# Kernel tuning notes

Measured on AMD Instinct MI355X. Metric: run time of the kernel, lower is better.

## Reference

```python
import jax, jax.numpy as jnp
import numpy as np

B, S, D, H = 4, 1024, 1024, 16
HD = D // H  # head_dim = 64


def setup_inputs() -> dict:
    key = jax.random.key(0)
    ks = jax.random.split(key, 12)
    std = 1.0 / np.sqrt(D)
    inp = {
        "query": jax.random.normal(ks[0], (B, S, D), jnp.float32),
        "key": jax.random.normal(ks[1], (B, S, D), jnp.float32),
        "value": jax.random.normal(ks[2], (B, S, D), jnp.float32),
        # four Linear(embed_dim, embed_dim) layers: q, k, v, out
        "Wq": jax.random.normal(ks[3], (D, D), jnp.float32) * std,
        "bq": jnp.zeros((D,), jnp.float32),
        "Wk": jax.random.normal(ks[4], (D, D), jnp.float32) * std,
        "bk": jnp.zeros((D,), jnp.float32),
        "Wv": jax.random.normal(ks[5], (D, D), jnp.float32) * std,
        "bv": jnp.zeros((D,), jnp.float32),
        "Wo": jax.random.normal(ks[6], (D, D), jnp.float32) * std,
        "bo": jnp.zeros((D,), jnp.float32),
        # compressor: Linear(num_heads, 1)
        "Wc": jax.random.normal(ks[7], (H,), jnp.float32) / np.sqrt(H),
        "bc": jnp.zeros((), jnp.float32),
    }
    return inp


def reference(query, key, value, Wq, bq, Wk, bk, Wv, bv, Wo, bo, Wc, bc):
    b, s, d = query.shape
    h, hd = H, HD

    def proj(x, W, bias):
        # [b,s,d] @ [d,d] -> [b,h,s,hd]
        y = jnp.einsum('bsd,de->bse', x, W) + bias
        return y.reshape(b, s, h, hd).transpose(0, 2, 1, 3)

    q = proj(query, Wq, bq)
    k = proj(key, Wk, bk)
    v = proj(value, Wv, bv)

    scores = jnp.einsum('bhqd,bhkd->bhqk', q, k) / np.sqrt(hd)
    p_attn = jax.nn.softmax(scores, axis=-1)  # [b,h,s,s]; dropout is identity in eval

    x = jnp.einsum('bhqk,bhkd->bhqd', p_attn, v)
    x = x.transpose(0, 2, 1, 3).reshape(b, s, d)
    out = jnp.einsum('bsd,de->bse', x, Wo) + bo

    # head compression: Linear(num_heads, 1) over head axis -> [b,1,s,s]
    attn_c = (jnp.einsum('bhqk,h->bqk', p_attn, Wc) + bc)[:, None, :, :]
    return out, attn_c
```

## Files before the change

### kernel.cpp

```cpp
#include <hip/hip_runtime.h>
#include <hip/hip_bf16.h>

#define SS 1024
#define DD 1024
#define HH 16
#define HDh 64

typedef short bf16x8 __attribute__((ext_vector_type(8)));
typedef float f32x4 __attribute__((ext_vector_type(4)));

__device__ inline unsigned short f2bf(float f) {
    union { __hip_bfloat16 h; unsigned short u; } cv;
    cv.h = __float2bfloat16(f);
    return cv.u;
}
__device__ inline float bf2f(short u) {
    unsigned int x = ((unsigned int)(unsigned short)u) << 16;
    return __uint_as_float(x);
}

#define PIN4(a, b, c, d) asm volatile("" : "+v"(a), "+v"(b), "+v"(c), "+v"(d))

__device__ inline void gload_lds16(const unsigned short* g, unsigned short* l) {
    __builtin_amdgcn_global_load_lds(
        (const __attribute__((address_space(1))) unsigned int*)g,
        (__attribute__((address_space(3))) unsigned int*)l, 16, 0, 0);
}

__global__ __launch_bounds__(256) void prep(
    const float* __restrict__ a, const float* __restrict__ b, const float* __restrict__ c,
    unsigned short* __restrict__ oa, unsigned short* __restrict__ ob, unsigned short* __restrict__ oc,
    const float* __restrict__ Wq, const float* __restrict__ Wk,
    const float* __restrict__ Wv, const float* __restrict__ Wo,
    unsigned short* __restrict__ oq, unsigned short* __restrict__ okk,
    unsigned short* __restrict__ ov, unsigned short* __restrict__ oo)
{
    __shared__ float tile[32][33];
    int bid = blockIdx.x;
    if (bid < 4096) {
        size_t i = ((size_t)bid * 256 + threadIdx.x) * 4;
        float4 va = *(const float4*)(a + i);
        float4 vb = *(const float4*)(b + i);
        float4 vc = *(const float4*)(c + i);
        *(ushort4*)(oa + i) = make_ushort4(f2bf(va.x), f2bf(va.y), f2bf(va.z), f2bf(va.w));
        *(ushort4*)(ob + i) = make_ushort4(f2bf(vb.x), f2bf(vb.y), f2bf(vb.z), f2bf(vb.w));
        *(ushort4*)(oc + i) = make_ushort4(f2bf(vc.x), f2bf(vc.y), f2bf(vc.z), f2bf(vc.w));
    } else {
        int idx = bid - 4096;
        int z = idx >> 10;
        const float* W = z == 0 ? Wq : (z == 1 ? Wk : (z == 2 ? Wv : Wo));
        unsigned short* O = z == 0 ? oq : (z == 1 ? okk : (z == 2 ? ov : oo));
        int e0 = (idx & 31) * 32, d0 = ((idx >> 5) & 31) * 32;
        int r = threadIdx.x >> 3, c4 = (threadIdx.x & 7) * 4;
        float4 v = *(const float4*)(W + (size_t)(d0 + r) * DD + e0 + c4);
        tile[r][c4 + 0] = v.x; tile[r][c4 + 1] = v.y; tile[r][c4 + 2] = v.z; tile[r][c4 + 3] = v.w;
        __syncthreads();
        ushort4 u = make_ushort4(f2bf(tile[c4 + 0][r]), f2bf(tile[c4 + 1][r]),
                                 f2bf(tile[c4 + 2][r]), f2bf(tile[c4 + 3][r]));
        *(ushort4*)(O + (size_t)(e0 + r) * DD + d0 + c4) = u;
    }
}

__device__ inline void gemm128_core(const unsigned short* __restrict__ A,
                                    const unsigned short* __restrict__ Bt,
                                    const float* __restrict__ bias,
                                    void* __restrict__ out, int mode, float oscale,
                                    int m0, int n0)
{
    __shared__ unsigned short As[128 * 64];
    __shared__ unsigned short Bs[128 * 64];
    int t = threadIdx.x;
    int w = t >> 6, lane = t & 63, quad = lane >> 4, l15 = lane & 15;
    int wm = w >> 1, wn = w & 1;

    f32x4 zero = {0.f, 0.f, 0.f, 0.f};
    f32x4 acc[4][4];
#pragma unroll
    for (int i = 0; i < 4; i++)
#pragma unroll
        for (int j = 0; j < 4; j++) acc[i][j] = zero;

    for (int k0 = 0; k0 < DD; k0 += 64) {
        __syncthreads();
#pragma unroll
        for (int i = 0; i < 8; i++) {
            int chunk = w + i * 4;
            int half = chunk >> 4;
            int sub = chunk & 15;
            const unsigned short* g = (half ? Bt : A)
                + (size_t)((half ? n0 : m0) + (sub >> 1) * 16 + (lane >> 2)) * DD
                + k0 + (sub & 1) * 32 + (lane & 3) * 8;
            unsigned short* l = (half ? Bs : As) + sub * 512 + lane * 8;
            gload_lds16(g, l);
        }
        __syncthreads();
#pragma unroll
        for (int kk = 0; kk < 2; kk++) {
            bf16x8 af[4], bfr[4];
#pragma unroll
            for (int mi = 0; mi < 4; mi++)
                af[mi] = *(const bf16x8*)&As[((wm * 4 + mi) * 2 + kk) * 512 + l15 * 32 + quad * 8];
#pragma unroll
            for (int ni = 0; ni < 4; ni++)
                bfr[ni] = *(const bf16x8*)&Bs[((wn * 4 + ni) * 2 + kk) * 512 + l15 * 32 + quad * 8];
#pragma unroll
            for (int mi = 0; mi < 4; mi++)
#pragma unroll
                for (int ni = 0; ni < 4; ni++)
                    acc[mi][ni] = __builtin_amdgcn_mfma_f32_16x16x32_bf16(af[mi], bfr[ni], acc[mi][ni], 0, 0, 0);
        }
    }

#pragma unroll
    for (int mi = 0; mi < 4; mi++)
#pragma unroll
        for (int ni = 0; ni < 4; ni++) {
            int n = n0 + wn * 64 + ni * 16 + l15;
            float bv = bias[n];
#pragma unroll
            for (int r = 0; r < 4; r++) {
                int m = m0 + wm * 64 + mi * 16 + quad * 4 + r;
                float v = (acc[mi][ni][r] + bv) * oscale;
                if (mode == 2) {
                    ((float*)out)[(size_t)m * DD + n] = v;
                } else {
                    int bb = m >> 10, s = m & 1023, hh = n >> 6, d = n & 63;
                    size_t head = (size_t)(bb * HH + hh) << 16;
                    size_t off;
                    if (mode == 0) {
                        off = head + (((size_t)(s >> 4) * 2 + (d >> 5)) * 64
                              + ((d >> 3) & 3) * 16 + (s & 15)) * 8 + (d & 7);
                    } else {
                        off = head + (((size_t)(s >> 5) * 4 + (d >> 4)) * 64
                              + ((s >> 3) & 3) * 16 + (d & 15)) * 8 + (s & 7);
                    }
                    ((unsigned short*)out)[off] = f2bf(v);
                }
            }
        }
}

#define SCLQ 0.18033688f

__global__ __launch_bounds__(256, 3) void gemm_qkv(
    const unsigned short* __restrict__ xq, const unsigned short* __restrict__ xk,
    const unsigned short* __restrict__ xv,
    const unsigned short* __restrict__ wtq, const unsigned short* __restrict__ wtk,
    const unsigned short* __restrict__ wtv,
    const float* __restrict__ bq, const float* __restrict__ bk, const float* __restrict__ bv,
    unsigned short* __restrict__ q, unsigned short* __restrict__ k, unsigned short* __restrict__ v)
{
    int bid = blockIdx.x;
    int swz = (bid & 7) * 96 + (bid >> 3);
    int z = swz >> 8, rem = swz & 255;
    int n0 = (rem & 7) * 128, m0 = (rem >> 3) * 128;
    const unsigned short* A  = z == 0 ? xq  : (z == 1 ? xk  : xv);
    const unsigned short* Bt = z == 0 ? wtq : (z == 1 ? wtk : wtv);
    const float* bias        = z == 0 ? bq  : (z == 1 ? bk  : bv);
    void* out                = z == 0 ? (void*)q : (z == 1 ? (void*)k : (void*)v);
    gemm128_core(A, Bt, bias, out, z == 2 ? 1 : 0, z == 0 ? SCLQ : 1.0f, m0, n0);
}

__global__ __launch_bounds__(256, 3) void gemm_o(
    const unsigned short* __restrict__ x, const unsigned short* __restrict__ wto,
    const float* __restrict__ bo, float* __restrict__ out)
{
    int bid = blockIdx.x;
    int swz = (bid & 7) * 32 + (bid >> 3);
    int n0 = (swz & 7) * 128, m0 = (swz >> 3) * 128;
    gemm128_core(x, wto, bo, out, 2, 1.0f, m0, n0);
}


__global__ __launch_bounds__(512, 4) void fattn_kernel(
    const unsigned short* __restrict__ qf, const unsigned short* __restrict__ kf,
    const unsigned short* __restrict__ vf, float* __restrict__ Z,
    unsigned short* __restrict__ xat)
{
    __shared__ __align__(16) unsigned short kls[2048];
    __shared__ __align__(16) unsigned short vls[2048];
    __shared__ __align__(16) unsigned short plds[8][640];
    int t = threadIdx.x, w = t >> 6, lane = t & 63, quad = lane >> 4, l15 = lane & 15;
    int bid = blockIdx.x;
    int swz = (bid & 7) * 64 + (bid >> 3);
    int bh = swz >> 3, m0 = (swz & 7) * 128;
    int b = bh >> 4, h = bh & 15;
    const unsigned short* qh = qf + ((size_t)bh << 16);
    const unsigned short* kh = kf + ((size_t)bh << 16);
    const unsigned short* vh = vf + ((size_t)bh << 16);

    bf16x8 qfrag[2];
    int s16b = (m0 >> 4) + w;
#pragma unroll
    for (int dh = 0; dh < 2; dh++)
        qfrag[dh] = *(const bf16x8*)(qh + (size_t)(s16b * 2 + dh) * 512 + lane * 8);

    f32x4 zero = {0.f, 0.f, 0.f, 0.f};
    f32x4 oacc[4];
#pragma unroll
    for (int ni = 0; ni < 4; ni++) oacc[ni] = zero;
    float zacc = 0.f;

    const unsigned short* ssrc = (w < 4 ? kh + (size_t)w * 512
                                        : vh + (size_t)(w - 4) * 512) + lane * 8;
    unsigned short* sdst = (w < 4 ? kls + w * 512 : vls + (w - 4) * 512) + lane * 8;

    for (int kt = 0; kt < 32; kt++) {
        __syncthreads();
        gload_lds16(ssrc + (size_t)kt * 2048, sdst);
        __syncthreads();

        bf16x8 kc[4], vc[4];
#pragma unroll
        for (int i = 0; i < 4; i++) {
            kc[i] = *(const bf16x8*)&kls[i * 512 + lane * 8];
            vc[i] = *(const bf16x8*)&vls[i * 512 + lane * 8];
        }

        f32x4 st[2];
#pragma unroll
        for (int si = 0; si < 2; si++) {
            st[si] = __builtin_amdgcn_mfma_f32_16x16x32_bf16(kc[si * 2 + 0], qfrag[0], zero, 0, 0, 0);
            st[si] = __builtin_amdgcn_mfma_f32_16x16x32_bf16(kc[si * 2 + 1], qfrag[1], st[si], 0, 0, 0);
        }

#pragma unroll
        for (int si = 0; si < 2; si++) {
            float p0 = exp2f(st[si][0]);
            float p1 = exp2f(st[si][1]);
            float p2 = exp2f(st[si][2]);
            float p3 = exp2f(st[si][3]);
            zacc += (p0 + p1) + (p2 + p3);
            unsigned int pk0 = (unsigned int)f2bf(p0) | ((unsigned int)f2bf(p1) << 16);
            unsigned int pk1 = (unsigned int)f2bf(p2) | ((unsigned int)f2bf(p3) << 16);
            *(uint2*)&plds[w][l15 * 40 + si * 16 + quad * 4] = make_uint2(pk0, pk1);
        }
        bf16x8 pa = *(const bf16x8*)&plds[w][l15 * 40 + quad * 8];

#pragma unroll
        for (int ni = 0; ni < 4; ni++)
            oacc[ni] = __builtin_amdgcn_mfma_f32_16x16x32_bf16(pa, vc[ni], oacc[ni], 0, 0, 0);
    }

    float zt = zacc;
    zt += __shfl_xor(zt, 16);
    zt += __shfl_xor(zt, 32);
    if (quad == 0)
        Z[(size_t)bh * 1024 + m0 + w * 16 + l15] = zt;

#pragma unroll
    for (int r = 0; r < 4; r++) {
        int qrow = quad * 4 + r;
        float iz = 1.f / __shfl(zt, qrow);
        int q = m0 + w * 16 + qrow;
#pragma unroll
        for (int ni = 0; ni < 4; ni++)
            xat[((size_t)(b * 1024 + q)) * 1024 + h * 64 + ni * 16 + l15] =
                f2bf(oacc[ni][r] * iz);
    }
}

__global__ __launch_bounds__(256, 3) void tail_kernel(
    const unsigned short* __restrict__ qf, const unsigned short* __restrict__ kf,
    const float* __restrict__ Z, const float* __restrict__ Wc,
    const float* __restrict__ bcp, float* __restrict__ attc,
    const unsigned short* __restrict__ xat, const unsigned short* __restrict__ wto,
    const float* __restrict__ bo, float* __restrict__ out0)
{
    if (blockIdx.x >= 512) {
        int bid2 = blockIdx.x - 512;
        int swz = (bid2 & 7) * 32 + (bid2 >> 3);
        int n0 = (swz & 7) * 128, m0 = (swz >> 3) * 128;
        gemm128_core(xat, wto, bo, out0, 2, 1.0f, m0, n0);
        return;
    }
    __shared__ unsigned short ks[2][8192];
    int t = threadIdx.x, w = t >> 6, lane = t & 63, quad = lane >> 4, l15 = lane & 15;
    int bid = blockIdx.x;
    int u = (bid & 7) * 64 + (bid >> 3);
    int kb = u & 7, qg = (u >> 3) & 15, b = u >> 7;
    int qt = qg * 4 + w;
    int q = qt * 16 + l15;
    float bc = *bcp;
    f32x4 zero = {0.f, 0.f, 0.f, 0.f};
    f32x4 acc[4][2];
#pragma unroll
    for (int kt = 0; kt < 4; kt++)
#pragma unroll
        for (int si = 0; si < 2; si++) acc[kt][si] = zero;

    float wzv[16];
#pragma unroll
    for (int h = 0; h < 16; h++)
        wzv[h] = Wc[h] / Z[(size_t)(b * 16 + h) * 1024 + q];

    {
        const unsigned short* src = kf + ((size_t)(b * 16) << 16) + (size_t)(kb * 16) * 512;
#pragma unroll
        for (int i = 0; i < 4; i++) {
            int c = w + i * 4;
            gload_lds16(src + (size_t)c * 512 + lane * 8, ks[0] + c * 512 + lane * 8);
        }
    }
    __syncthreads();

    int cb = 0;
    for (int h = 0; h < 16; h++) {
        int bh = b * 16 + h;
        const unsigned short* qh = qf + ((size_t)bh << 16);
        bf16x8 qfr0 = *(const bf16x8*)(qh + (size_t)(qt * 2 + 0) * 512 + lane * 8);
        bf16x8 qfr1 = *(const bf16x8*)(qh + (size_t)(qt * 2 + 1) * 512 + lane * 8);
        if (h < 15) {
            const unsigned short* src = kf + ((size_t)(bh + 1) << 16) + (size_t)(kb * 16) * 512;
#pragma unroll
            for (int i = 0; i < 4; i++) {
                int c = w + i * 4;
                gload_lds16(src + (size_t)c * 512 + lane * 8, ks[cb ^ 1] + c * 512 + lane * 8);
            }
        }
        float wz = wzv[h];
#pragma unroll
        for (int kt = 0; kt < 4; kt++) {
            bf16x8 kfr[4];
#pragma unroll
            for (int i = 0; i < 4; i++)
                kfr[i] = *(const bf16x8*)&ks[cb][(size_t)(kt * 4 + i) * 512 + lane * 8];
#pragma unroll
            for (int si = 0; si < 2; si++) {
                f32x4 st = __builtin_amdgcn_mfma_f32_16x16x32_bf16(kfr[si * 2 + 0], qfr0, zero, 0, 0, 0);
                st = __builtin_amdgcn_mfma_f32_16x16x32_bf16(kfr[si * 2 + 1], qfr1, st, 0, 0, 0);
#pragma unroll
                for (int r = 0; r < 4; r++)
                    acc[kt][si][r] += wz * exp2f(st[r]);
            }
        }
        __syncthreads();
        cb ^= 1;
    }
#pragma unroll
    for (int kt = 0; kt < 4; kt++)
#pragma unroll
        for (int si = 0; si < 2; si++) {
            float4 vv = make_float4(acc[kt][si][0] + bc, acc[kt][si][1] + bc,
                                    acc[kt][si][2] + bc, acc[kt][si][3] + bc);
            *(float4*)(attc + ((size_t)(b * 1024 + q)) * 1024 + kb * 128 + kt * 32 + si * 16 + quad * 4) = vv;
        }
}

#define LDK(f) (*(const bf16x8*)(kh + ((size_t)(f) * 64 + lane) * 8))
#define LDV(f) (*(const bf16x8*)(vh + ((size_t)(f) * 64 + lane) * 8))

__global__ __launch_bounds__(1024, 4) void attn_kernel(
    const unsigned short* __restrict__ qf, const unsigned short* __restrict__ kf,
    const unsigned short* __restrict__ vf, const float* __restrict__ Wc,
    const float* __restrict__ bcp, unsigned short* __restrict__ xout,
    float* __restrict__ attc)
{
    __shared__ float accc[16][1028];
    __shared__ unsigned short tsc[16][16][36];

    int t = threadIdx.x, w = t >> 6, lane = t & 63, quad = lane >> 4, l15 = lane & 15;
    int b = blockIdx.x >> 6, qt = blockIdx.x & 63;
    int h = w;

    for (int i = t; i < 16 * 1028; i += 1024) (&accc[0][0])[i] = 0.f;
    __syncthreads();

    const unsigned short* qh = qf + ((size_t)(b * HH + h) << 16);
    const unsigned short* kh = kf + ((size_t)(b * HH + h) << 16);
    const unsigned short* vh = vf + ((size_t)(b * HH + h) << 16);
    float wc = Wc[h], bc = *bcp;
    f32x4 zero = {0.f, 0.f, 0.f, 0.f};

    bf16x8 a0 = *(const bf16x8*)(qh + ((size_t)(qt * 2 + 0) * 64 + lane) * 8);
    bf16x8 a1 = *(const bf16x8*)(qh + ((size_t)(qt * 2 + 1) * 64 + lane) * 8);

    float rs[4] = {0.f, 0.f, 0.f, 0.f};
    bf16x8 c0 = LDK(0), c1 = LDK(1), c2 = LDK(2), c3 = LDK(3);
    PIN4(c0, c1, c2, c3);
    bf16x8 d0 = LDK(4), d1 = LDK(5), d2 = LDK(6), d3 = LDK(7);
    PIN4(d0, d1, d2, d3);
#pragma unroll 2
    for (int g = 0; g < 32; g++) {
        int gn = g < 30 ? g + 2 : 31;
        bf16x8 n0 = LDK(gn * 4 + 0), n1 = LDK(gn * 4 + 1);
        bf16x8 n2 = LDK(gn * 4 + 2), n3 = LDK(gn * 4 + 3);
        PIN4(n0, n1, n2, n3);
        f32x4 s0 = zero, s1 = zero;
        s0 = __builtin_amdgcn_mfma_f32_16x16x32_bf16(a0, c0, s0, 0, 0, 0);
        s0 = __builtin_amdgcn_mfma_f32_16x16x32_bf16(a1, c1, s0, 0, 0, 0);
        s1 = __builtin_amdgcn_mfma_f32_16x16x32_bf16(a0, c2, s1, 0, 0, 0);
        s1 = __builtin_amdgcn_mfma_f32_16x16x32_bf16(a1, c3, s1, 0, 0, 0);
#pragma unroll
        for (int r = 0; r < 4; r++) rs[r] += exp2f(s0[r]) + exp2f(s1[r]);
        c0 = d0; c1 = d1; c2 = d2; c3 = d3;
        d0 = n0; d1 = n1; d2 = n2; d3 = n3;
    }
#pragma unroll
    for (int r = 0; r < 4; r++) {
        rs[r] += __shfl_xor(rs[r], 1);
        rs[r] += __shfl_xor(rs[r], 2);
        rs[r] += __shfl_xor(rs[r], 4);
        rs[r] += __shfl_xor(rs[r], 8);
    }
    float invC[4], sC[4];
#pragma unroll
    for (int r = 0; r < 4; r++) { invC[r] = 1.f / rs[r]; sC[r] = wc * invC[r]; }

    f32x4 o0 = zero, o1 = zero, o2 = zero, o3 = zero;
    int cc0 = (2 * w) & 31;
    bf16x8 k0 = LDK(cc0 * 4 + 0), k1 = LDK(cc0 * 4 + 1);
    bf16x8 k2 = LDK(cc0 * 4 + 2), k3 = LDK(cc0 * 4 + 3);
    PIN4(k0, k1, k2, k3);
    bf16x8 v0 = LDV(cc0 * 4 + 0), v1 = LDV(cc0 * 4 + 1);
    bf16x8 v2 = LDV(cc0 * 4 + 2), v3 = LDV(cc0 * 4 + 3);
    PIN4(v0, v1, v2, v3);
#pragma unroll 2
    for (int i = 0; i < 32; i++) {
        int cc = (i + 2 * w) & 31;
        int cn = ((i + 1) + 2 * w) & 31;
        bf16x8 kn0 = LDK(cn * 4 + 0), kn1 = LDK(cn * 4 + 1);
        bf16x8 kn2 = LDK(cn * 4 + 2), kn3 = LDK(cn * 4 + 3);
        PIN4(kn0, kn1, kn2, kn3);
        bf16x8 vn0 = LDV(cn * 4 + 0), vn1 = LDV(cn * 4 + 1);
        bf16x8 vn2 = LDV(cn * 4 + 2), vn3 = LDV(cn * 4 + 3);
        PIN4(vn0, vn1, vn2, vn3);

        f32x4 s0 = zero, s1 = zero;
        s0 = __builtin_amdgcn_mfma_f32_16x16x32_bf16(a0, k0, s0, 0, 0, 0);
        s0 = __builtin_amdgcn_mfma_f32_16x16x32_bf16(a1, k1, s0, 0, 0, 0);
        s1 = __builtin_amdgcn_mfma_f32_16x16x32_bf16(a0, k2, s1, 0, 0, 0);
        s1 = __builtin_amdgcn_mfma_f32_16x16x32_bf16(a1, k3, s1, 0, 0, 0);

#pragma unroll
        for (int r = 0; r < 4; r++) {
            float p0 = exp2f(s0[r]);
            float p1 = exp2f(s1[r]);
            int row = quad * 4 + r;
            tsc[w][row][l15] = f2bf(p0);
            tsc[w][row][16 + l15] = f2bf(p1);
            atomicAdd(&accc[row][cc * 32 + l15], sC[r] * p0);
            atomicAdd(&accc[row][cc * 32 + 16 + l15], sC[r] * p1);
        }
        bf16x8 ap = *(const bf16x8*)&tsc[w][l15][quad * 8];

        o0 = __builtin_amdgcn_mfma_f32_16x16x32_bf16(ap, v0, o0, 0, 0, 0);
        o1 = __builtin_amdgcn_mfma_f32_16x16x32_bf16(ap, v1, o1, 0, 0, 0);
        o2 = __builtin_amdgcn_mfma_f32_16x16x32_bf16(ap, v2, o2, 0, 0, 0);
        o3 = __builtin_amdgcn_mfma_f32_16x16x32_bf16(ap, v3, o3, 0, 0, 0);
        k0 = kn0; k1 = kn1; k2 = kn2; k3 = kn3;
        v0 = vn0; v1 = vn1; v2 = vn2; v3 = vn3;
    }

    f32x4 oo[4] = {o0, o1, o2, o3};
#pragma unroll
    for (int j = 0; j < 4; j++)
#pragma unroll
        for (int r = 0; r < 4; r++) {
            int row = quad * 4 + r;
            xout[((size_t)(b * SS) + qt * 16 + row) * DD + h * 64 + j * 16 + l15] =
                f2bf(oo[j][r] * invC[r]);
        }

    __syncthreads();
    for (int i = t; i < 16 * 1024; i += 1024) {
        int row = i >> 10, col = i & 1023;
        attc[((size_t)b * SS + qt * 16 + row) * SS + col] = accc[row][col] + bc;
    }
}

extern "C" void kernel_launch(void* const* d_in, const int* in_sizes, int n_in,
                              void* d_out, int out_size, void* d_ws, size_t ws_size,
                              hipStream_t stream) {
    const float* query = (const float*)d_in[0];
    const float* key   = (const float*)d_in[1];
    const float* value = (const float*)d_in[2];
    const float* Wq = (const float*)d_in[3];
    const float* bq = (const float*)d_in[4];
    const float* Wk = (const float*)d_in[5];
    const float* bk = (const float*)d_in[6];
    const float* Wv = (const float*)d_in[7];
    const float* bv = (const float*)d_in[8];
    const float* Wo = (const float*)d_in[9];
    const float* bo = (const float*)d_in[10];
    const float* Wc = (const float*)d_in[11];
    const float* bc = (const float*)d_in[12];

    unsigned short* ws  = (unsigned short*)d_ws;
    unsigned short* xq  = ws;
    unsigned short* xk  = xq  + (size_t)4194304;
    unsigned short* xv  = xk  + (size_t)4194304;
    unsigned short* wtq = xv  + (size_t)4194304;
    unsigned short* wtk = wtq + (size_t)1048576;
    unsigned short* wtv = wtk + (size_t)1048576;
    unsigned short* wto = wtv + (size_t)1048576;
    unsigned short* qfb = wto + (size_t)1048576;
    unsigned short* kfb = qfb + (size_t)4194304;
    unsigned short* vfb = kfb + (size_t)4194304;
    unsigned short* xat = vfb + (size_t)4194304;

    float* out0 = (float*)d_out;
    float* attc = out0 + (size_t)4194304;

    const size_t base_bytes = 67108864;
    const size_t z_bytes = 262144;
    bool fast = ws_size >= base_bytes + z_bytes;

    hipLaunchKernelGGL(prep, dim3(8192), dim3(256), 0, stream,
                       query, key, value, xq, xk, xv,
                       Wq, Wk, Wv, Wo, wtq, wtk, wtv, wto);
    hipLaunchKernelGGL(gemm_qkv, dim3(768), dim3(256), 0, stream,
                       xq, xk, xv, wtq, wtk, wtv, bq, bk, bv, qfb, kfb, vfb);

    if (fast) {
        float* Zbuf = (float*)((char*)d_ws + base_bytes);
        hipLaunchKernelGGL(fattn_kernel, dim3(512), dim3(512), 0, stream,
                           qfb, kfb, vfb, Zbuf, xat);
        hipLaunchKernelGGL(tail_kernel, dim3(768), dim3(256), 0, stream,
                           qfb, kfb, Zbuf, Wc, bc, attc,
                           xat, wto, bo, out0);
    } else {
        hipLaunchKernelGGL(attn_kernel, dim3(256), dim3(1024), 0, stream,
                           qfb, kfb, vfb, Wc, bc, xat, attc);
        hipLaunchKernelGGL(gemm_o, dim3(256), dim3(256), 0, stream,
                           xat, wto, bo, out0);
    }
}
```

Baseline: 246.2 us.

## Double-buffer K/V tiles in attention and use BK=32 for output GEMM

The attention kernel now double-buffers its K/V LDS tiles, prefetching the next tile during compute and cutting the barriers per iteration from two to one. The output projection GEMM, including the copy fused into the tail kernel, is templated to use a 32-wide K step, halving its LDS footprint so more blocks can be resident. The cost is extra LDS in the attention kernel and twice as many K iterations (and barriers) in the output GEMM.

```diff
diff --git a/kernel.cpp b/kernel.cpp
--- a/kernel.cpp
+++ b/kernel.cpp
@@ -61,14 +61,15 @@
     }
 }
 
+template<int BK>
 __device__ inline void gemm128_core(const unsigned short* __restrict__ A,
                                     const unsigned short* __restrict__ Bt,
                                     const float* __restrict__ bias,
                                     void* __restrict__ out, int mode, float oscale,
                                     int m0, int n0)
 {
-    __shared__ unsigned short As[128 * 64];
-    __shared__ unsigned short Bs[128 * 64];
+    __shared__ unsigned short As[128 * BK];
+    __shared__ unsigned short Bs[128 * BK];
     int t = threadIdx.x;
     int w = t >> 6, lane = t & 63, quad = lane >> 4, l15 = lane & 15;
     int wm = w >> 1, wn = w & 1;
@@ -80,34 +81,62 @@
 #pragma unroll
         for (int j = 0; j < 4; j++) acc[i][j] = zero;
 
-    for (int k0 = 0; k0 < DD; k0 += 64) {
+    for (int k0 = 0; k0 < DD; k0 += BK) {
         __syncthreads();
-#pragma unroll
-        for (int i = 0; i < 8; i++) {
-            int chunk = w + i * 4;
-            int half = chunk >> 4;
-            int sub = chunk & 15;
-            const unsigned short* g = (half ? Bt : A)
-                + (size_t)((half ? n0 : m0) + (sub >> 1) * 16 + (lane >> 2)) * DD
-                + k0 + (sub & 1) * 32 + (lane & 3) * 8;
-            unsigned short* l = (half ? Bs : As) + sub * 512 + lane * 8;
-            gload_lds16(g, l);
+        if constexpr (BK == 32) {
+#pragma unroll
+            for (int i = 0; i < 4; i++) {
+                int chunk = w + i * 4;
+                int half = chunk >> 3;
+                int c = chunk & 7;
+                const unsigned short* g = (half ? Bt : A)
+                    + (size_t)((half ? n0 : m0) + c * 16 + (lane >> 2)) * DD + k0 + (lane & 3) * 8;
+                unsigned short* l = (half ? Bs : As) + c * 512 + lane * 8;
+                gload_lds16(g, l);
+            }
+        } else {
+#pragma unroll
+            for (int i = 0; i < 8; i++) {
+                int chunk = w + i * 4;
+                int half = chunk >> 4;
+                int sub = chunk & 15;
+                const unsigned short* g = (half ? Bt : A)
+                    + (size_t)((half ? n0 : m0) + (sub >> 1) * 16 + (lane >> 2)) * DD
+                    + k0 + (sub & 1) * 32 + (lane & 3) * 8;
+                unsigned short* l = (half ? Bs : As) + sub * 512 + lane * 8;
+                gload_lds16(g, l);
+            }
         }
         __syncthreads();
-#pragma unroll
-        for (int kk = 0; kk < 2; kk++) {
+        if constexpr (BK == 32) {
             bf16x8 af[4], bfr[4];
 #pragma unroll
             for (int mi = 0; mi < 4; mi++)
-                af[mi] = *(const bf16x8*)&As[((wm * 4 + mi) * 2 + kk) * 512 + l15 * 32 + quad * 8];
+                af[mi] = *(const bf16x8*)&As[(wm * 64 + mi * 16 + l15) * 32 + quad * 8];
 #pragma unroll
             for (int ni = 0; ni < 4; ni++)
-                bfr[ni] = *(const bf16x8*)&Bs[((wn * 4 + ni) * 2 + kk) * 512 + l15 * 32 + quad * 8];
+                bfr[ni] = *(const bf16x8*)&Bs[(wn * 64 + ni * 16 + l15) * 32 + quad * 8];
 #pragma unroll
             for (int mi = 0; mi < 4; mi++)
 #pragma unroll
                 for (int ni = 0; ni < 4; ni++)
                     acc[mi][ni] = __builtin_amdgcn_mfma_f32_16x16x32_bf16(af[mi], bfr[ni], acc[mi][ni], 0, 0, 0);
+        } else {
+#pragma unroll
+            for (int kk = 0; kk < 2; kk++) {
+                bf16x8 af[4], bfr[4];
+#pragma unroll
+                for (int mi = 0; mi < 4; mi++)
+                    af[mi] = *(const bf16x8*)&As[((wm * 4 + mi) * 2 + kk) * 512 + l15 * 32 + quad * 8];
+#pragma unroll
+                for (int ni = 0; ni < 4; ni++)
+                    bfr[ni] = *(const bf16x8*)&Bs[((wn * 4 + ni) * 2 + kk) * 512 + l15 * 32 + quad * 8];
+#pragma unroll
+                for (int mi = 0; mi < 4; mi++)
+#pragma unroll
+                    for (int ni = 0; ni < 4; ni++)
+                        acc[mi][ni] = __builtin_amdgcn_mfma_f32_16x16x32_bf16(af[mi], bfr[ni], acc[mi][ni], 0, 0, 0);
+            }
         }
     }
 
@@ -158,7 +187,7 @@
     const unsigned short* Bt = z == 0 ? wtq : (z == 1 ? wtk : wtv);
     const float* bias        = z == 0 ? bq  : (z == 1 ? bk  : bv);
     void* out                = z == 0 ? (void*)q : (z == 1 ? (void*)k : (void*)v);
-    gemm128_core(A, Bt, bias, out, z == 2 ? 1 : 0, z == 0 ? SCLQ : 1.0f, m0, n0);
+    gemm128_core<64>(A, Bt, bias, out, z == 2 ? 1 : 0, z == 0 ? SCLQ : 1.0f, m0, n0);
 }
 
 __global__ __launch_bounds__(256, 3) void gemm_o(
@@ -168,7 +197,7 @@
     int bid = blockIdx.x;
     int swz = (bid & 7) * 32 + (bid >> 3);
     int n0 = (swz & 7) * 128, m0 = (swz >> 3) * 128;
-    gemm128_core(x, wto, bo, out, 2, 1.0f, m0, n0);
+    gemm128_core<32>(x, wto, bo, out, 2, 1.0f, m0, n0);
 }
 
 
@@ -177,8 +206,8 @@
     const unsigned short* __restrict__ vf, float* __restrict__ Z,
     unsigned short* __restrict__ xat)
 {
-    __shared__ __align__(16) unsigned short kls[2048];
-    __shared__ __align__(16) unsigned short vls[2048];
+    __shared__ __align__(16) unsigned short kls[2][2048];
+    __shared__ __align__(16) unsigned short vls[2][2048];
     __shared__ __align__(16) unsigned short plds[8][640];
     int t = threadIdx.x, w = t >> 6, lane = t & 63, quad = lane >> 4, l15 = lane & 15;
     int bid = blockIdx.x;
@@ -203,18 +232,22 @@
 
     const unsigned short* ssrc = (w < 4 ? kh + (size_t)w * 512
                                         : vh + (size_t)(w - 4) * 512) + lane * 8;
-    unsigned short* sdst = (w < 4 ? kls + w * 512 : vls + (w - 4) * 512) + lane * 8;
-
+    int sinner = (w < 4 ? w * 512 : (w - 4) * 512) + lane * 8;
+
+    gload_lds16(ssrc, (w < 4 ? kls[0] : vls[0]) + sinner);
+    __syncthreads();
+
+    int cur = 0;
     for (int kt = 0; kt < 32; kt++) {
-        __syncthreads();
-        gload_lds16(ssrc + (size_t)kt * 2048, sdst);
-        __syncthreads();
+        if (kt < 31)
+            gload_lds16(ssrc + (size_t)(kt + 1) * 2048,
+                        (w < 4 ? kls[cur ^ 1] : vls[cur ^ 1]) + sinner);
 
         bf16x8 kc[4], vc[4];
 #pragma unroll
         for (int i = 0; i < 4; i++) {
-            kc[i] = *(const bf16x8*)&kls[i * 512 + lane * 8];
-            vc[i] = *(const bf16x8*)&vls[i * 512 + lane * 8];
+            kc[i] = *(const bf16x8*)&kls[cur][i * 512 + lane * 8];
+            vc[i] = *(const bf16x8*)&vls[cur][i * 512 + lane * 8];
         }
 
         f32x4 st[2];
@@ -240,6 +273,9 @@
 #pragma unroll
         for (int ni = 0; ni < 4; ni++)
             oacc[ni] = __builtin_amdgcn_mfma_f32_16x16x32_bf16(pa, vc[ni], oacc[ni], 0, 0, 0);
+
+        __syncthreads();
+        cur ^= 1;
     }
 
     float zt = zacc;
@@ -271,7 +307,7 @@
         int bid2 = blockIdx.x - 512;
         int swz = (bid2 & 7) * 32 + (bid2 >> 3);
         int n0 = (swz & 7) * 128, m0 = (swz >> 3) * 128;
-        gemm128_core(xat, wto, bo, out0, 2, 1.0f, m0, n0);
+        gemm128_core<32>(xat, wto, bo, out0, 2, 1.0f, m0, n0);
         return;
     }
     __shared__ unsigned short ks[2][8192];
```

Result: faster. 225.3 us (-8.5%).
